# Optimization experiments

Hardware: AMD Instinct MI355X
Metric: run time of the kernel (lower is better)

The kernel has to match this reference:

```python
import jax, jax.numpy as jnp
import numpy as np

B, L, H, E = 4, 2048, 8, 64

def setup_inputs() -> dict:
    key = jax.random.key(0)
    kq, kk, kv = jax.random.split(key, 3)
    queries = jax.random.normal(kq, (B, L, H, E), dtype=jnp.float32)
    keys = jax.random.normal(kk, (B, L, H, E), dtype=jnp.float32)
    values = jax.random.normal(kv, (B, L, H, E), dtype=jnp.float32)
    return {"queries": queries, "keys": keys, "values": values}

def reference(queries, keys, values):
    # queries/keys/values: [B, L, H, E]
    E_ = queries.shape[-1]
    scale = 1.0 / jnp.sqrt(jnp.float32(E_))
    # scores: [B, H, L, S]
    scores = jnp.einsum('blhe,bshe->bhls', queries, keys)
    Lq, S = scores.shape[-2], scores.shape[-1]
    # TriangularCausalMask: mask positions where s > l (strict upper triangle)
    causal = jnp.tril(jnp.ones((Lq, S), dtype=bool))
    scores = jnp.where(causal, scores, -jnp.inf)
    A = jax.nn.softmax(scale * scores, axis=-1)  # dropout p=0 -> identity
    V = jnp.einsum('bhls,bshd->blhd', A, values)
    return V
```

## Files before the change

### kernel.cpp

```cpp
#include <hip/hip_runtime.h>
#include <hip/hip_bf16.h>


#define Bc 4
#define Lc 2048
#define Hc 8
#define Ec 64
#define TB 64
#define NT (Lc / TB)
#define BH_BYTES (NT * TB * Ec * 2)
#define WS_V_OFF ((size_t)32 * BH_BYTES)

using f32x4 = __attribute__((ext_vector_type(4))) float;
using f16x8 = __attribute__((ext_vector_type(8))) _Float16;
using f16x4 = __attribute__((ext_vector_type(4))) _Float16;
using hf16x2 = __fp16 __attribute__((ext_vector_type(2)));

static __device__ __forceinline__ unsigned int pk2(float lo, float hi) {
    union { hf16x2 h; unsigned int u; } c;
    c.h = __builtin_amdgcn_cvt_pkrtz(lo, hi);
    return c.u;
}

static __device__ __forceinline__ void gload16(const void* g, void* l) {
    __builtin_amdgcn_global_load_lds(
        (const __attribute__((address_space(1))) unsigned int*)g,
        (__attribute__((address_space(3))) unsigned int*)l, 16, 0, 0);
}

__global__ __launch_bounds__(256)
void prep_kernel(const float* __restrict__ K, const float* __restrict__ V,
                 char* __restrict__ ws)
{
    __shared__ char vstage[64 * 144];

    const int bid = blockIdx.x;
    const int bh = bid >> 5, kt = bid & 31;
    const int b = bh >> 3, h = bh & 7;
    const int tid = threadIdx.x;
    const int r = tid >> 2, q4 = tid & 3;
    const int c0 = 16 * q4;
    const size_t base_bh = (size_t)b * Lc * Hc * Ec + (size_t)h * Ec;
    const int kbase = kt * TB;
    char* kimg = ws + (size_t)bh * BH_BYTES + (size_t)kt * 8192;
    char* vimg = ws + WS_V_OFF + (size_t)bh * BH_BYTES + (size_t)kt * 8192;

    const int rs = (r & 7) << 4;
    {
        const float* kp = K + base_bh + (size_t)(kbase + r) * 512 + c0;
        unsigned int w[8];
        #pragma unroll
        for (int i = 0; i < 4; ++i) {
            float4 f = *(const float4*)(kp + 4 * i);
            w[2*i]   = pk2(f.x, f.y);
            w[2*i+1] = pk2(f.z, f.w);
        }
        *(uint4*)(kimg + r * 128 + ((32*q4)      ^ rs)) = *(uint4*)&w[0];
        *(uint4*)(kimg + r * 128 + ((32*q4 + 16) ^ rs)) = *(uint4*)&w[4];
    }
    {
        const float* vp = V + base_bh + (size_t)(kbase + r) * 512 + c0;
        unsigned int w[8];
        #pragma unroll
        for (int i = 0; i < 4; ++i) {
            float4 f = *(const float4*)(vp + 4 * i);
            w[2*i]   = pk2(f.x, f.y);
            w[2*i+1] = pk2(f.z, f.w);
        }
        *(uint4*)(vstage + r * 144 + 32*q4)      = *(uint4*)&w[0];
        *(uint4*)(vstage + r * 144 + 32*q4 + 16) = *(uint4*)&w[4];
    }
    __syncthreads();
    {
        const int e = tid >> 2, kq = tid & 3, kv0 = 16 * kq;
        unsigned int w[8];
        #pragma unroll
        for (int i = 0; i < 8; ++i) {
            unsigned int lo = *(const unsigned short*)(vstage + (kv0 + 2*i)     * 144 + 2*e);
            unsigned int hi = *(const unsigned short*)(vstage + (kv0 + 2*i + 1) * 144 + 2*e);
            w[i] = lo | (hi << 16);
        }
        const int es = (e & 7) << 4;
        *(uint4*)(vimg + e * 128 + ((32*kq)      ^ es)) = *(uint4*)&w[0];
        *(uint4*)(vimg + e * 128 + ((32*kq + 16) ^ es)) = *(uint4*)&w[4];
    }
}

__global__ __launch_bounds__(256)
void fa_fwd_kernel(const float* __restrict__ Q, const char* __restrict__ ws,
                   float* __restrict__ Out)
{
    __shared__ char klds[2 * 8192];
    __shared__ char vlds[2 * 8192];

    const int bid = blockIdx.x;
    const int pi  = bid >> 5;
    const int bh  = bid & 31;
    const int b   = bh >> 3, h = bh & 7;

    const int tid  = threadIdx.x;
    const int wid  = tid >> 6;
    const int lane = tid & 63;
    const int l15  = lane & 15;
    const int l4   = lane >> 4;

    const size_t base_bh = (size_t)b * Lc * Hc * Ec + (size_t)h * Ec;
    const char* kimg = ws + (size_t)bh * BH_BYTES;
    const char* vimg = ws + WS_V_OFF + (size_t)bh * BH_BYTES;
    const float SL2E = 0.125f * 1.44269504088896340736f;

    const int sw  = (l15 & 7) << 4;
    const int ko0 = l15 * 128 + ((16 * l4)      ^ sw);
    const int ko1 = l15 * 128 + ((64 + 16 * l4) ^ sw);
    int vo[4];
    #pragma unroll
    for (int m = 0; m < 4; ++m) vo[m] = l15 * 128 + ((32 * m + 8 * l4) ^ sw);

    f16x4 ones;
    {
        const _Float16 ov = (_Float16)((l15 == 0) ? 1.0f : 0.0f);
        ones[0] = ov; ones[1] = ov; ones[2] = ov; ones[3] = ov;
    }

    const int stoff = wid * 2048 + lane * 16;

    #pragma unroll 1
    for (int half = 0; half < 2; ++half) {
        const int qt = half ? pi : (NT - 1 - pi);
        const int qrow0 = qt * TB + 16 * wid;

        f16x8 qa0, qa1;
        {
            const float* qpr = Q + base_bh + (size_t)(qrow0 + l15) * 512 + 8 * l4;
            float4 f0 = *(const float4*)(qpr);
            float4 f1 = *(const float4*)(qpr + 4);
            float4 f2 = *(const float4*)(qpr + 32);
            float4 f3 = *(const float4*)(qpr + 36);
            union { f16x8 v; unsigned int u[4]; } pk;
            pk.u[0] = pk2(f0.x * SL2E, f0.y * SL2E);
            pk.u[1] = pk2(f0.z * SL2E, f0.w * SL2E);
            pk.u[2] = pk2(f1.x * SL2E, f1.y * SL2E);
            pk.u[3] = pk2(f1.z * SL2E, f1.w * SL2E);
            qa0 = pk.v;
            pk.u[0] = pk2(f2.x * SL2E, f2.y * SL2E);
            pk.u[1] = pk2(f2.z * SL2E, f2.w * SL2E);
            pk.u[2] = pk2(f3.x * SL2E, f3.y * SL2E);
            pk.u[3] = pk2(f3.z * SL2E, f3.w * SL2E);
            qa1 = pk.v;
        }

        f32x4 o[4] = {};
        f32x4 ol = {};
        float m_run = -1e30f;

        gload16(kimg + stoff,        klds + stoff);
        gload16(kimg + stoff + 1024, klds + stoff + 1024);
        gload16(vimg + stoff,        vlds + stoff);
        gload16(vimg + stoff + 1024, vlds + stoff + 1024);
        __syncthreads();

        for (int kt = 0; kt <= qt; ++kt) {
            const int cur = kt & 1;
            const char* kb = klds + cur * 8192;
            const char* vb = vlds + cur * 8192;

            if (kt < qt) {
                const char* ks = kimg + (size_t)(kt + 1) * 8192;
                const char* vs = vimg + (size_t)(kt + 1) * 8192;
                char* kd = klds + (cur ^ 1) * 8192;
                char* vd = vlds + (cur ^ 1) * 8192;
                gload16(ks + stoff,        kd + stoff);
                gload16(ks + stoff + 1024, kd + stoff + 1024);
                gload16(vs + stoff,        vd + stoff);
                gload16(vs + stoff + 1024, vd + stoff + 1024);
            }

            f32x4 s[4];
            #pragma unroll
            for (int n = 0; n < 4; ++n) {
                f16x8 a0 = *(const f16x8*)(kb + n * 2048 + ko0);
                f16x8 a1 = *(const f16x8*)(kb + n * 2048 + ko1);
                f32x4 z = {0.f, 0.f, 0.f, 0.f};
                z = __builtin_amdgcn_mfma_f32_16x16x32_f16(a0, qa0, z, 0, 0, 0);
                z = __builtin_amdgcn_mfma_f32_16x16x32_f16(a1, qa1, z, 0, 0, 0);
                s[n] = z;
            }

            if (kt == qt) {
                const int q_g = qrow0 + l15;
                #pragma unroll
                for (int n = 0; n < 4; ++n) {
                    #pragma unroll
                    for (int r = 0; r < 4; ++r) {
                        const int kv_g = kt * TB + 16 * n + 4 * l4 + r;
                        if (kv_g > q_g) s[n][r] = -1e30f;
                    }
                }
            }

            float a0 = fmaxf(s[0][0], s[0][1]), a1 = fmaxf(s[0][2], s[0][3]);
            float a2 = fmaxf(s[1][0], s[1][1]), a3 = fmaxf(s[1][2], s[1][3]);
            float a4 = fmaxf(s[2][0], s[2][1]), a5 = fmaxf(s[2][2], s[2][3]);
            float a6 = fmaxf(s[3][0], s[3][1]), a7 = fmaxf(s[3][2], s[3][3]);
            float pmax = fmaxf(fmaxf(fmaxf(a0, a1), fmaxf(a2, a3)),
                               fmaxf(fmaxf(a4, a5), fmaxf(a6, a7)));
            pmax = fmaxf(pmax, __shfl_xor(pmax, 16, 64));
            pmax = fmaxf(pmax, __shfl_xor(pmax, 32, 64));

            if (!__all(pmax - m_run <= 8.0f)) {
                const float m_new = fmaxf(m_run, pmax);
                const float fac = __builtin_exp2f(m_run - m_new);
                m_run = m_new;
                float fr[4];
                #pragma unroll
                for (int r = 0; r < 4; ++r) fr[r] = __shfl(fac, 4 * l4 + r, 64);
                #pragma unroll
                for (int c = 0; c < 4; ++c)
                    #pragma unroll
                    for (int r = 0; r < 4; ++r) o[c][r] *= fr[r];
                #pragma unroll
                for (int r = 0; r < 4; ++r) ol[r] *= fr[r];
            }

            unsigned int ph[4][2];
            #pragma unroll
            for (int n = 0; n < 4; ++n) {
                float p0 = __builtin_exp2f(s[n][0] - m_run);
                float p1 = __builtin_exp2f(s[n][1] - m_run);
                float p2 = __builtin_exp2f(s[n][2] - m_run);
                float p3 = __builtin_exp2f(s[n][3] - m_run);
                ph[n][0] = pk2(p0, p1);
                ph[n][1] = pk2(p2, p3);
            }

            #pragma unroll
            for (int m = 0; m < 4; ++m) {
                union { f16x4 h; unsigned int u[2]; } pa;
                pa.u[0] = ph[m][0]; pa.u[1] = ph[m][1];
                ol = __builtin_amdgcn_mfma_f32_16x16x16f16(pa.h, ones, ol, 0, 0, 0);
                #pragma unroll
                for (int c = 0; c < 4; ++c) {
                    const f16x4 vbf = *(const f16x4*)(vb + c * 2048 + vo[m]);
                    o[c] = __builtin_amdgcn_mfma_f32_16x16x16f16(pa.h, vbf, o[c], 0, 0, 0);
                }
            }
            __syncthreads();
        }

        float ir[4];
        #pragma unroll
        for (int r = 0; r < 4; ++r) {
            const float iv = 1.0f / ol[r];
            ir[r] = __shfl(iv, 16 * l4, 64);
        }
        float* op = Out + base_bh;
        #pragma unroll
        for (int c = 0; c < 4; ++c)
            #pragma unroll
            for (int r = 0; r < 4; ++r)
                op[(size_t)(qrow0 + 4 * l4 + r) * 512 + 16 * c + l15] = o[c][r] * ir[r];
    }
}

extern "C" void kernel_launch(void* const* d_in, const int* in_sizes, int n_in,
                              void* d_out, int out_size, void* d_ws, size_t ws_size,
                              hipStream_t stream) {
    const float* Q = (const float*)d_in[0];
    const float* K = (const float*)d_in[1];
    const float* V = (const float*)d_in[2];
    float* O = (float*)d_out;
    char* ws = (char*)d_ws;
    hipLaunchKernelGGL(prep_kernel, dim3(Bc * Hc * NT), dim3(256), 0, stream, K, V, ws);
    hipLaunchKernelGGL(fa_fwd_kernel, dim3((NT / 2) * Bc * Hc), dim3(256), 0, stream, Q, ws, O);
}
```

Measured before the change: 65.50 us.

## Use 2-wave blocks with 32 query rows per wave, one q-tile per block

The block drops from 4 waves to 2. Each wave now handles two 16-row query groups, so every K/V fragment read from LDS feeds twice as many MFMAs. The paired causal scheduling (one long and one short q-tile per block) is replaced by one q-tile per block across a grid twice as large, ordered longest-first. This targets LDS read traffic per MFMA and the serial two-half loop, at the cost of more registers per thread, fewer threads to issue the K/V staging loads, and a different load-balance pattern.

```diff
diff --git a/kernel.cpp b/kernel.cpp
--- a/kernel.cpp
+++ b/kernel.cpp
@@ -86,7 +86,7 @@
     }
 }
 
-__global__ __launch_bounds__(256)
+__global__ __launch_bounds__(128, 3)
 void fa_fwd_kernel(const float* __restrict__ Q, const char* __restrict__ ws,
                    float* __restrict__ Out)
 {
@@ -94,9 +94,11 @@
     __shared__ char vlds[2 * 8192];
 
     const int bid = blockIdx.x;
-    const int pi  = bid >> 5;
+    const int qi  = bid >> 5;
     const int bh  = bid & 31;
     const int b   = bh >> 3, h = bh & 7;
+    const int qt  = (NT - 1) - qi;
+    const int qbase = qt * TB;
 
     const int tid  = threadIdx.x;
     const int wid  = tid >> 6;
@@ -122,143 +124,167 @@
         ones[0] = ov; ones[1] = ov; ones[2] = ov; ones[3] = ov;
     }
 
-    const int stoff = wid * 2048 + lane * 16;
-
-    #pragma unroll 1
-    for (int half = 0; half < 2; ++half) {
-        const int qt = half ? pi : (NT - 1 - pi);
-        const int qrow0 = qt * TB + 16 * wid;
-
-        f16x8 qa0, qa1;
-        {
-            const float* qpr = Q + base_bh + (size_t)(qrow0 + l15) * 512 + 8 * l4;
-            float4 f0 = *(const float4*)(qpr);
-            float4 f1 = *(const float4*)(qpr + 4);
-            float4 f2 = *(const float4*)(qpr + 32);
-            float4 f3 = *(const float4*)(qpr + 36);
-            union { f16x8 v; unsigned int u[4]; } pk;
-            pk.u[0] = pk2(f0.x * SL2E, f0.y * SL2E);
-            pk.u[1] = pk2(f0.z * SL2E, f0.w * SL2E);
-            pk.u[2] = pk2(f1.x * SL2E, f1.y * SL2E);
-            pk.u[3] = pk2(f1.z * SL2E, f1.w * SL2E);
-            qa0 = pk.v;
-            pk.u[0] = pk2(f2.x * SL2E, f2.y * SL2E);
-            pk.u[1] = pk2(f2.z * SL2E, f2.w * SL2E);
-            pk.u[2] = pk2(f3.x * SL2E, f3.y * SL2E);
-            pk.u[3] = pk2(f3.z * SL2E, f3.w * SL2E);
-            qa1 = pk.v;
-        }
-
-        f32x4 o[4] = {};
-        f32x4 ol = {};
-        float m_run = -1e30f;
-
-        gload16(kimg + stoff,        klds + stoff);
-        gload16(kimg + stoff + 1024, klds + stoff + 1024);
-        gload16(vimg + stoff,        vlds + stoff);
-        gload16(vimg + stoff + 1024, vlds + stoff + 1024);
-        __syncthreads();
-
-        for (int kt = 0; kt <= qt; ++kt) {
-            const int cur = kt & 1;
-            const char* kb = klds + cur * 8192;
-            const char* vb = vlds + cur * 8192;
-
-            if (kt < qt) {
-                const char* ks = kimg + (size_t)(kt + 1) * 8192;
-                const char* vs = vimg + (size_t)(kt + 1) * 8192;
-                char* kd = klds + (cur ^ 1) * 8192;
-                char* vd = vlds + (cur ^ 1) * 8192;
-                gload16(ks + stoff,        kd + stoff);
-                gload16(ks + stoff + 1024, kd + stoff + 1024);
-                gload16(vs + stoff,        vd + stoff);
-                gload16(vs + stoff + 1024, vd + stoff + 1024);
-            }
-
-            f32x4 s[4];
-            #pragma unroll
-            for (int n = 0; n < 4; ++n) {
-                f16x8 a0 = *(const f16x8*)(kb + n * 2048 + ko0);
-                f16x8 a1 = *(const f16x8*)(kb + n * 2048 + ko1);
+    const int stoff = tid * 16;
+
+    f16x8 qa[2][2];
+    #pragma unroll
+    for (int g = 0; g < 2; ++g) {
+        const int qrow = qbase + 32 * wid + 16 * g + l15;
+        const float* qpr = Q + base_bh + (size_t)qrow * 512 + 8 * l4;
+        float4 f0 = *(const float4*)(qpr);
+        float4 f1 = *(const float4*)(qpr + 4);
+        float4 f2 = *(const float4*)(qpr + 32);
+        float4 f3 = *(const float4*)(qpr + 36);
+        union { f16x8 v; unsigned int u[4]; } pk;
+        pk.u[0] = pk2(f0.x * SL2E, f0.y * SL2E);
+        pk.u[1] = pk2(f0.z * SL2E, f0.w * SL2E);
+        pk.u[2] = pk2(f1.x * SL2E, f1.y * SL2E);
+        pk.u[3] = pk2(f1.z * SL2E, f1.w * SL2E);
+        qa[g][0] = pk.v;
+        pk.u[0] = pk2(f2.x * SL2E, f2.y * SL2E);
+        pk.u[1] = pk2(f2.z * SL2E, f2.w * SL2E);
+        pk.u[2] = pk2(f3.x * SL2E, f3.y * SL2E);
+        pk.u[3] = pk2(f3.z * SL2E, f3.w * SL2E);
+        qa[g][1] = pk.v;
+    }
+
+    f32x4 o[2][4] = {};
+    f32x4 ol[2] = {};
+    float m_run[2] = {-1e30f, -1e30f};
+
+    #pragma unroll
+    for (int j = 0; j < 4; ++j) {
+        gload16(kimg + stoff + j * 2048, klds + stoff + j * 2048);
+        gload16(vimg + stoff + j * 2048, vlds + stoff + j * 2048);
+    }
+    __syncthreads();
+
+    for (int kt = 0; kt <= qt; ++kt) {
+        const int cur = kt & 1;
+        const char* kb = klds + cur * 8192;
+        const char* vb = vlds + cur * 8192;
+
+        if (kt < qt) {
+            const char* ks = kimg + (size_t)(kt + 1) * 8192;
+            const char* vs = vimg + (size_t)(kt + 1) * 8192;
+            char* kd = klds + (cur ^ 1) * 8192;
+            char* vd = vlds + (cur ^ 1) * 8192;
+            #pragma unroll
+            for (int j = 0; j < 4; ++j) {
+                gload16(ks + stoff + j * 2048, kd + stoff + j * 2048);
+                gload16(vs + stoff + j * 2048, vd + stoff + j * 2048);
+            }
+        }
+
+        f32x4 s[2][4];
+        #pragma unroll
+        for (int n = 0; n < 4; ++n) {
+            f16x8 a0 = *(const f16x8*)(kb + n * 2048 + ko0);
+            f16x8 a1 = *(const f16x8*)(kb + n * 2048 + ko1);
+            #pragma unroll
+            for (int g = 0; g < 2; ++g) {
                 f32x4 z = {0.f, 0.f, 0.f, 0.f};
-                z = __builtin_amdgcn_mfma_f32_16x16x32_f16(a0, qa0, z, 0, 0, 0);
-                z = __builtin_amdgcn_mfma_f32_16x16x32_f16(a1, qa1, z, 0, 0, 0);
-                s[n] = z;
-            }
-
-            if (kt == qt) {
-                const int q_g = qrow0 + l15;
+                z = __builtin_amdgcn_mfma_f32_16x16x32_f16(a0, qa[g][0], z, 0, 0, 0);
+                z = __builtin_amdgcn_mfma_f32_16x16x32_f16(a1, qa[g][1], z, 0, 0, 0);
+                s[g][n] = z;
+            }
+        }
+
+        if (kt == qt) {
+            #pragma unroll
+            for (int g = 0; g < 2; ++g) {
+                const int q_g = qbase + 32 * wid + 16 * g + l15;
                 #pragma unroll
                 for (int n = 0; n < 4; ++n) {
                     #pragma unroll
                     for (int r = 0; r < 4; ++r) {
                         const int kv_g = kt * TB + 16 * n + 4 * l4 + r;
-                        if (kv_g > q_g) s[n][r] = -1e30f;
+                        if (kv_g > q_g) s[g][n][r] = -1e30f;
                     }
                 }
             }
-
-            float a0 = fmaxf(s[0][0], s[0][1]), a1 = fmaxf(s[0][2], s[0][3]);
-            float a2 = fmaxf(s[1][0], s[1][1]), a3 = fmaxf(s[1][2], s[1][3]);
-            float a4 = fmaxf(s[2][0], s[2][1]), a5 = fmaxf(s[2][2], s[2][3]);
-            float a6 = fmaxf(s[3][0], s[3][1]), a7 = fmaxf(s[3][2], s[3][3]);
-            float pmax = fmaxf(fmaxf(fmaxf(a0, a1), fmaxf(a2, a3)),
-                               fmaxf(fmaxf(a4, a5), fmaxf(a6, a7)));
-            pmax = fmaxf(pmax, __shfl_xor(pmax, 16, 64));
-            pmax = fmaxf(pmax, __shfl_xor(pmax, 32, 64));
-
-            if (!__all(pmax - m_run <= 8.0f)) {
-                const float m_new = fmaxf(m_run, pmax);
-                const float fac = __builtin_exp2f(m_run - m_new);
-                m_run = m_new;
+        }
+
+        float pmax[2];
+        #pragma unroll
+        for (int g = 0; g < 2; ++g) {
+            float a0 = fmaxf(s[g][0][0], s[g][0][1]), a1 = fmaxf(s[g][0][2], s[g][0][3]);
+            float a2 = fmaxf(s[g][1][0], s[g][1][1]), a3 = fmaxf(s[g][1][2], s[g][1][3]);
+            float a4 = fmaxf(s[g][2][0], s[g][2][1]), a5 = fmaxf(s[g][2][2], s[g][2][3]);
+            float a6 = fmaxf(s[g][3][0], s[g][3][1]), a7 = fmaxf(s[g][3][2], s[g][3][3]);
+            float pm = fmaxf(fmaxf(fmaxf(a0, a1), fmaxf(a2, a3)),
+                             fmaxf(fmaxf(a4, a5), fmaxf(a6, a7)));
+            pm = fmaxf(pm, __shfl_xor(pm, 16, 64));
+            pm = fmaxf(pm, __shfl_xor(pm, 32, 64));
+            pmax[g] = pm;
+        }
+
+        #pragma unroll
+        for (int g = 0; g < 2; ++g) {
+            if (!__all(pmax[g] - m_run[g] <= 8.0f)) {
+                const float m_new = fmaxf(m_run[g], pmax[g]);
+                const float fac = __builtin_exp2f(m_run[g] - m_new);
+                m_run[g] = m_new;
                 float fr[4];
                 #pragma unroll
                 for (int r = 0; r < 4; ++r) fr[r] = __shfl(fac, 4 * l4 + r, 64);
                 #pragma unroll
                 for (int c = 0; c < 4; ++c)
                     #pragma unroll
-                    for (int r = 0; r < 4; ++r) o[c][r] *= fr[r];
-                #pragma unroll
-                for (int r = 0; r < 4; ++r) ol[r] *= fr[r];
-            }
-
-            unsigned int ph[4][2];
+                    for (int r = 0; r < 4; ++r) o[g][c][r] *= fr[r];
+                #pragma unroll
+                for (int r = 0; r < 4; ++r) ol[g][r] *= fr[r];
+            }
+        }
+
+        unsigned int ph[2][4][2];
+        #pragma unroll
+        for (int g = 0; g < 2; ++g) {
             #pragma unroll
             for (int n = 0; n < 4; ++n) {
-                float p0 = __builtin_exp2f(s[n][0] - m_run);
-                float p1 = __builtin_exp2f(s[n][1] - m_run);
-                float p2 = __builtin_exp2f(s[n][2] - m_run);
-                float p3 = __builtin_exp2f(s[n][3] - m_run);
-                ph[n][0] = pk2(p0, p1);
-                ph[n][1] = pk2(p2, p3);
-            }
-
-            #pragma unroll
-            for (int m = 0; m < 4; ++m) {
+                float p0 = __builtin_exp2f(s[g][n][0] - m_run[g]);
+                float p1 = __builtin_exp2f(s[g][n][1] - m_run[g]);
+                float p2 = __builtin_exp2f(s[g][n][2] - m_run[g]);
+                float p3 = __builtin_exp2f(s[g][n][3] - m_run[g]);
+                ph[g][n][0] = pk2(p0, p1);
+                ph[g][n][1] = pk2(p2, p3);
+            }
+        }
+
+        #pragma unroll
+        for (int m = 0; m < 4; ++m) {
+            f16x4 vbf[4];
+            #pragma unroll
+            for (int c = 0; c < 4; ++c)
+                vbf[c] = *(const f16x4*)(vb + c * 2048 + vo[m]);
+            #pragma unroll
+            for (int g = 0; g < 2; ++g) {
                 union { f16x4 h; unsigned int u[2]; } pa;
-                pa.u[0] = ph[m][0]; pa.u[1] = ph[m][1];
-                ol = __builtin_amdgcn_mfma_f32_16x16x16f16(pa.h, ones, ol, 0, 0, 0);
-                #pragma unroll
-                for (int c = 0; c < 4; ++c) {
-                    const f16x4 vbf = *(const f16x4*)(vb + c * 2048 + vo[m]);
-                    o[c] = __builtin_amdgcn_mfma_f32_16x16x16f16(pa.h, vbf, o[c], 0, 0, 0);
-                }
-            }
-            __syncthreads();
-        }
-
+                pa.u[0] = ph[g][m][0]; pa.u[1] = ph[g][m][1];
+                ol[g] = __builtin_amdgcn_mfma_f32_16x16x16f16(pa.h, ones, ol[g], 0, 0, 0);
+                #pragma unroll
+                for (int c = 0; c < 4; ++c)
+                    o[g][c] = __builtin_amdgcn_mfma_f32_16x16x16f16(pa.h, vbf[c], o[g][c], 0, 0, 0);
+            }
+        }
+        __syncthreads();
+    }
+
+    float* op = Out + base_bh;
+    #pragma unroll
+    for (int g = 0; g < 2; ++g) {
         float ir[4];
         #pragma unroll
         for (int r = 0; r < 4; ++r) {
-            const float iv = 1.0f / ol[r];
+            const float iv = 1.0f / ol[g][r];
             ir[r] = __shfl(iv, 16 * l4, 64);
         }
-        float* op = Out + base_bh;
+        const int qrow0 = qbase + 32 * wid + 16 * g;
         #pragma unroll
         for (int c = 0; c < 4; ++c)
             #pragma unroll
             for (int r = 0; r < 4; ++r)
-                op[(size_t)(qrow0 + 4 * l4 + r) * 512 + 16 * c + l15] = o[c][r] * ir[r];
+                op[(size_t)(qrow0 + 4 * l4 + r) * 512 + 16 * c + l15] = o[g][c][r] * ir[r];
     }
 }
 
@@ -271,5 +297,5 @@
     float* O = (float*)d_out;
     char* ws = (char*)d_ws;
     hipLaunchKernelGGL(prep_kernel, dim3(Bc * Hc * NT), dim3(256), 0, stream, K, V, ws);
-    hipLaunchKernelGGL(fa_fwd_kernel, dim3((NT / 2) * Bc * Hc), dim3(256), 0, stream, Q, ws, O);
-}
+    hipLaunchKernelGGL(fa_fwd_kernel, dim3(NT * Bc * Hc), dim3(128), 0, stream, Q, ws, O);
+}
```

Result: slower. 73.30 us (+11.9%).
